# Performance work log

Hardware: AMD Instinct MI355X
Metric: run time of the kernel (lower is better)

The kernel has to match this reference:

```python
import jax, jax.numpy as jnp
import numpy as np

N, E, B = 25600, 307200, 256
H, D, F0, K = 256, 16, 7, 6
GNN_OUT, TDA_IN, TDA_OUT, MEG_IN, MEG_OUT = 192, 32, 128, 16, 64
FUSION = GNN_OUT + TDA_OUT + MEG_OUT  # 384
MID = FUSION // 2  # 192


def _ln(x, g, b, eps=1e-5):
    m = x.mean(-1, keepdims=True)
    v = x.var(-1, keepdims=True)
    return (x - m) * jax.lax.rsqrt(v + eps) * g + b


def _ntn(x, pos, neg):
    return jnp.nan_to_num(x, nan=0.0, posinf=pos, neginf=neg)


def setup_inputs():
    key = jax.random.key(0)
    ks = iter(jax.random.split(key, 80))
    p = lambda *s: 0.05 * jax.random.normal(next(ks), s, jnp.float32)
    inp = {
        "x": jax.random.normal(next(ks), (N, F0), jnp.float32),
        "edge_attr": jax.random.uniform(next(ks), (E, D), dtype=jnp.float32),
        "tda": jax.random.normal(next(ks), (B, TDA_IN), jnp.float32),
        "megnet": jax.random.normal(next(ks), (B, MEG_IN), jnp.float32),
        "edge_index": jax.random.randint(next(ks), (2, E), 0, N),
        "batch": jnp.repeat(jnp.arange(B), N // B),
        # GNN encoder
        "gin_W": p(F0, H), "gin_b": jnp.zeros(H),
        "conv_Wf": p(6, 2 * H + D, H), "conv_bf": jnp.zeros((6, H)),
        "conv_Ws": p(6, 2 * H + D, H), "conv_bs": jnp.zeros((6, H)),
        "gln_g": jnp.ones((6, H)), "gln_b": jnp.zeros((6, H)),
        "gout_W": p(H, GNN_OUT), "gout_b": jnp.zeros(GNN_OUT),
        # TDA projector 32->256->256->128
        "t1_W": p(TDA_IN, 2 * TDA_OUT), "t1_b": jnp.zeros(2 * TDA_OUT),
        "tln1_g": jnp.ones(2 * TDA_OUT), "tln1_b": jnp.zeros(2 * TDA_OUT),
        "t2_W": p(2 * TDA_OUT, 2 * TDA_OUT), "t2_b": jnp.zeros(2 * TDA_OUT),
        "tln2_g": jnp.ones(2 * TDA_OUT), "tln2_b": jnp.zeros(2 * TDA_OUT),
        "t3_W": p(2 * TDA_OUT, TDA_OUT), "t3_b": jnp.zeros(TDA_OUT),
        # MEGNet projector 16->128->128->64
        "m1_W": p(MEG_IN, 2 * MEG_OUT), "m1_b": jnp.zeros(2 * MEG_OUT),
        "mln1_g": jnp.ones(2 * MEG_OUT), "mln1_b": jnp.zeros(2 * MEG_OUT),
        "m2_W": p(2 * MEG_OUT, 2 * MEG_OUT), "m2_b": jnp.zeros(2 * MEG_OUT),
        "mln2_g": jnp.ones(2 * MEG_OUT), "mln2_b": jnp.zeros(2 * MEG_OUT),
        "m3_W": p(2 * MEG_OUT, MEG_OUT), "m3_b": jnp.zeros(MEG_OUT),
        # fusion LN
        "fln_g": jnp.ones(FUSION), "fln_b": jnp.zeros(FUSION),
        # CPPN gate 384->48->24->6
        "g1_W": p(FUSION, K * 8), "g1_b": jnp.zeros(K * 8),
        "hln_g": jnp.ones(K * 8), "hln_b": jnp.zeros(K * 8),
        "g2_W": p(K * 8, K * 4), "g2_b": jnp.zeros(K * 4),
        "g3_W": p(K * 4, K), "g3_b": jnp.zeros(K),
        # CPPN poly branches stacked over K
        "plin_W": p(K, FUSION), "plin_b": jnp.zeros(K),
        "pq1_W": p(K, FUSION, MID), "pq1_b": jnp.zeros((K, MID)),
        "pq2_W": p(K, MID), "pq2_b": jnp.zeros(K),
        "pc1_W": p(K, FUSION, MID // 2), "pc1_b": jnp.zeros((K, MID // 2)),
        "pc2_W": p(K, MID // 2), "pc2_b": jnp.zeros(K),
    }
    return inp


def _forward(x, edge_attr, tda, megnet, edge_index, batch,
             gin_W, gin_b, conv_Wf, conv_bf, conv_Ws, conv_bs, gln_g, gln_b, gout_W, gout_b,
             t1_W, t1_b, tln1_g, tln1_b, t2_W, t2_b, tln2_g, tln2_b, t3_W, t3_b,
             m1_W, m1_b, mln1_g, mln1_b, m2_W, m2_b, mln2_g, mln2_b, m3_W, m3_b,
             fln_g, fln_b,
             g1_W, g1_b, hln_g, hln_b, g2_W, g2_b, g3_W, g3_b,
             plin_W, plin_b, pq1_W, pq1_b, pq2_W, pq2_b, pc1_W, pc1_b, pc2_W, pc2_b):
    silu = jax.nn.silu
    tda = _ntn(tda, 3.0, -3.0)
    megnet = _ntn(megnet, 3.0, -3.0)
    x = _ntn(x, 3.0, -3.0)
    ea = _ntn(edge_attr, 1.0, 0.0)
    src, dst = edge_index[0], edge_index[1]

    h = silu(x @ gin_W + gin_b)  # [N, H]
    for i in range(6):
        # CGConv message: z_ij = [x_i, x_j, e_ij]; sigmoid(z Wf) * softplus(z Ws); sum-agg + root
        z = jnp.concatenate([h[dst], h[src], ea], axis=-1)  # [E, 2H+D]
        msg = jax.nn.sigmoid(z @ conv_Wf[i] + conv_bf[i]) * jax.nn.softplus(z @ conv_Ws[i] + conv_bs[i])
        conv = h + jax.ops.segment_sum(msg, dst, num_segments=N)
        h = _ln(silu(conv) + h, gln_g[i], gln_b[i])
    cnt = jax.ops.segment_sum(jnp.ones((N, 1), h.dtype), batch, num_segments=B)
    pooled = jax.ops.segment_sum(h, batch, num_segments=B) / jnp.maximum(cnt, 1.0)
    z_gnn = jnp.nan_to_num(pooled @ gout_W + gout_b)  # [B, 192]

    # --- projectors ---
    a = _ln(silu(tda @ t1_W + t1_b), tln1_g, tln1_b)
    a = _ln(silu(a @ t2_W + t2_b), tln2_g, tln2_b)
    z_tda = jnp.nan_to_num(a @ t3_W + t3_b)  # [B, 128]
    m = _ln(silu(megnet @ m1_W + m1_b), mln1_g, mln1_b)
    m = _ln(silu(m @ m2_W + m2_b), mln2_g, mln2_b)
    z_meg = jnp.nan_to_num(m @ m3_W + m3_b)  # [B, 64]

    z = _ln(jnp.concatenate([z_gnn, z_tda, z_meg], axis=-1), fln_g, fln_b)  # [B, 384]

    # --- CPPN mixture head ---
    g = _ln(silu(z @ g1_W + g1_b), hln_g, hln_b)
    g = silu(g @ g2_W + g2_b)
    gates = jax.nn.softmax(g @ g3_W + g3_b, axis=-1)  # [B, K]
    lin = jnp.einsum('bd,kd->bk', z, plin_W) + plin_b
    hq = silu(jnp.einsum('bd,kdm->bkm', z, pq1_W) + pq1_b)  # [B, K, 192]
    q = jnp.einsum('bkm,km->bk', hq, pq2_W) + pq2_b
    hc = silu(jnp.einsum('bd,kdm->bkm', z, pc1_W) + pc1_b) ** 2  # [B, K, 96]
    c = jnp.einsum('bkm,km->bk', hc, pc2_W) + pc2_b
    y = (gates * (lin + q + c)).sum(-1)  # [B]
    return y, z


def reference(x, edge_attr, tda, megnet, edge_index, batch,
              gin_W, gin_b, conv_Wf, conv_bf, conv_Ws, conv_bs, gln_g, gln_b, gout_W, gout_b,
              t1_W, t1_b, tln1_g, tln1_b, t2_W, t2_b, tln2_g, tln2_b, t3_W, t3_b,
              m1_W, m1_b, mln1_g, mln1_b, m2_W, m2_b, mln2_g, mln2_b, m3_W, m3_b,
              fln_g, fln_b,
              g1_W, g1_b, hln_g, hln_b, g2_W, g2_b, g3_W, g3_b,
              plin_W, plin_b, pq1_W, pq1_b, pq2_W, pq2_b, pc1_W, pc1_b, pc2_W, pc2_b):
    return _forward(x, edge_attr, tda, megnet, edge_index, batch,
                    gin_W, gin_b, conv_Wf, conv_bf, conv_Ws, conv_bs, gln_g, gln_b, gout_W, gout_b,
                    t1_W, t1_b, tln1_g, tln1_b, t2_W, t2_b, tln2_g, tln2_b, t3_W, t3_b,
                    m1_W, m1_b, mln1_g, mln1_b, m2_W, m2_b, mln2_g, mln2_b, m3_W, m3_b,
                    fln_g, fln_b,
                    g1_W, g1_b, hln_g, hln_b, g2_W, g2_b, g3_W, g3_b,
                    plin_W, plin_b, pq1_W, pq1_b, pq2_W, pq2_b, pc1_W, pc1_b, pc2_W, pc2_b)
```

## Files before the change

### kernel.cpp

```cpp
#include <hip/hip_runtime.h>
#include <hip/hip_bf16.h>
#include <cmath>

#define NN 25600
#define NE 307200
#define NB 256
#define HD 256

typedef __attribute__((ext_vector_type(8))) short short8;
typedef __attribute__((ext_vector_type(4))) float f32x4;
typedef __attribute__((ext_vector_type(2))) float f32x2;

__device__ __forceinline__ float ntn_f(float v, float pos, float neg) {
  if (isnan(v)) return 0.f;
  if (isinf(v)) return v > 0.f ? pos : neg;
  return v;
}
__device__ __forceinline__ float ntn_def(float v) {
  if (isnan(v)) return 0.f;
  if (isinf(v)) return v > 0.f ? 3.4028234663852886e38f : -3.4028234663852886e38f;
  return v;
}
__device__ __forceinline__ float sigmoid_f(float x) { return 1.f / (1.f + __expf(-x)); }
__device__ __forceinline__ float silu_f(float x) { return x * sigmoid_f(x); }
__device__ __forceinline__ float softplus_f(float x) {
  return fmaxf(x, 0.f) + __logf(1.f + __expf(-fabsf(x)));
}
__device__ __forceinline__ unsigned short f2bf(float f) {
  unsigned int u = __float_as_uint(f);
  u += 0x7fffu + ((u >> 16) & 1u);
  return (unsigned short)(u >> 16);
}
__device__ __forceinline__ f32x2 bfpair(unsigned int u) {
  f32x2 r;
  r.x = __uint_as_float(u << 16);
  r.y = __uint_as_float(u & 0xffff0000u);
  return r;
}

template <int NW>
__device__ __forceinline__ float blockSum(float v, float* sred) {
  int lane = threadIdx.x & 63, w = threadIdx.x >> 6;
#pragma unroll
  for (int o = 32; o; o >>= 1) v += __shfl_xor(v, o);
  __syncthreads();
  if (lane == 0) sred[w] = v;
  __syncthreads();
  float r = 0.f;
#pragma unroll
  for (int i = 0; i < NW; ++i) r += sred[i];
  return r;
}

__global__ void k_hist(const int* __restrict__ dst, int* __restrict__ counts, int E) {
  int e = blockIdx.x * 256 + threadIdx.x;
  if (e < E) atomicAdd(&counts[dst[e]], 1);
}

__global__ __launch_bounds__(1024) void k_scan(const int* __restrict__ counts,
                                               int* __restrict__ offs, int n) {
  __shared__ int sd[1024];
  __shared__ int run;
  int tid = threadIdx.x;
  if (tid == 0) run = 0;
  __syncthreads();
  for (int base = 0; base < n; base += 1024) {
    int i = base + tid;
    int v = (i < n) ? counts[i] : 0;
    sd[tid] = v;
    __syncthreads();
    int acc = v;
    for (int off = 1; off < 1024; off <<= 1) {
      int t = (tid >= off) ? sd[tid - off] : 0;
      __syncthreads();
      acc += t;
      sd[tid] = acc;
      __syncthreads();
    }
    int r = run;
    if (i < n) offs[i] = r + acc - v;
    __syncthreads();
    if (tid == 1023) run = r + sd[1023];
    __syncthreads();
  }
  if (threadIdx.x == 0) offs[n] = run;
}

__global__ void k_scatter(const int* __restrict__ dst, const int* __restrict__ offs,
                          int* __restrict__ cursor, int* __restrict__ eidx, int E) {
  int e = blockIdx.x * 256 + threadIdx.x;
  if (e < E) {
    int d = dst[e];
    int p = offs[d] + atomicAdd(&cursor[d], 1);
    eidx[p] = e;
  }
}

__global__ void k_srcperm(const int* __restrict__ eidx, const int* __restrict__ srcArr,
                          int* __restrict__ srcs, int E) {
  int i = blockIdx.x * 256 + threadIdx.x;
  if (i < E) srcs[i] = srcArr[eidx[i]];
}

__global__ void k_eaperm(const int* __restrict__ eidx, const float* __restrict__ ea,
                         float* __restrict__ eacsr, int E) {
  int gid = blockIdx.x * 256 + threadIdx.x;
  if (gid < E * 16) {
    int ii = gid >> 4, k = gid & 15;
    eacsr[gid] = ea[(size_t)eidx[ii] * 16 + k];
  }
}

__global__ void k_pack(const float* __restrict__ conv_Wf, const float* __restrict__ conv_Ws,
                       unsigned short* __restrict__ w4t) {
  int layer = blockIdx.y;
  int gid = blockIdx.x * 256 + threadIdx.x;
  int k = gid & 255;
  int c = gid >> 8;
  int j = c & 255;
  int tbl = c >> 8;
  const float* W = (tbl < 2) ? conv_Wf : conv_Ws;
  int krow = (tbl & 1) ? 256 + k : k;
  float v = W[((size_t)layer * 528 + krow) * 256 + j];
  w4t[((size_t)layer * 1024 + c) * 256 + k] = f2bf(v);
}

__global__ void k_gin(const float* __restrict__ x, const float* __restrict__ W,
                      const float* __restrict__ bias, float* __restrict__ h,
                      unsigned short* __restrict__ hbf) {
  int n = blockIdx.x, j = threadIdx.x;
  float xv[7];
#pragma unroll
  for (int k = 0; k < 7; ++k) xv[k] = ntn_f(x[n * 7 + k], 3.f, -3.f);
  float acc = bias[j];
#pragma unroll
  for (int k = 0; k < 7; ++k) acc += xv[k] * W[k * 256 + j];
  float o = silu_f(acc);
  h[(size_t)n * 256 + j] = o;
  hbf[(size_t)n * 256 + j] = f2bf(o);
}

__global__ __launch_bounds__(256) void k_gemm_bf16(
    const unsigned short* __restrict__ Abf,
    const unsigned short* __restrict__ w4t,
    const float* __restrict__ bf, const float* __restrict__ bs,
    unsigned short* __restrict__ Pout) {
  __shared__ unsigned short As[128 * 56];
  __shared__ unsigned short Bs[128 * 56];
  int tid = threadIdx.x;
  int lane = tid & 63, w = tid >> 6;
  int wr = w >> 1, wc = w & 1;
  int m0 = blockIdx.x * 128, n0 = blockIdx.y * 128;
  int l15 = lane & 15, l4 = lane >> 4;
  f32x4 acc[4][4];
#pragma unroll
  for (int i = 0; i < 4; ++i)
#pragma unroll
    for (int j = 0; j < 4; ++j) acc[i][j] = (f32x4)0.f;
  for (int kt = 0; kt < 8; ++kt) {
    int k0 = kt * 32;
    if (kt) __syncthreads();
#pragma unroll
    for (int c = 0; c < 2; ++c) {
      int chunk = tid + c * 256;
      int row = chunk >> 2, q = chunk & 3;
      *(uint4*)&As[row * 56 + q * 8] =
          *(const uint4*)&Abf[(size_t)(m0 + row) * 256 + k0 + q * 8];
      *(uint4*)&Bs[row * 56 + q * 8] =
          *(const uint4*)&w4t[(size_t)(n0 + row) * 256 + k0 + q * 8];
    }
    __syncthreads();
    short8 a[4], b[4];
#pragma unroll
    for (int f = 0; f < 4; ++f) {
      a[f] = *(const short8*)&As[(wr * 64 + f * 16 + l15) * 56 + l4 * 8];
      b[f] = *(const short8*)&Bs[(wc * 64 + f * 16 + l15) * 56 + l4 * 8];
    }
#pragma unroll
    for (int i = 0; i < 4; ++i)
#pragma unroll
      for (int j = 0; j < 4; ++j)
        acc[i][j] = __builtin_amdgcn_mfma_f32_16x16x32_bf16(a[i], b[j], acc[i][j], 0, 0, 0);
  }
#pragma unroll
  for (int j = 0; j < 4; ++j) {
    int gcol = n0 + wc * 64 + j * 16 + l15;
    float bias = (gcol < 256) ? bf[gcol] : (gcol >= 512 && gcol < 768) ? bs[gcol - 512] : 0.f;
#pragma unroll
    for (int i = 0; i < 4; ++i) {
#pragma unroll
      for (int r = 0; r < 4; ++r) {
        int grow = m0 + wr * 64 + i * 16 + l4 * 4 + r;
        Pout[(size_t)grow * 1024 + gcol] = f2bf(acc[i][j][r] + bias);
      }
    }
  }
}

__global__ __launch_bounds__(256, 2) void k_edge(
    const float* __restrict__ h, const unsigned short* __restrict__ P,
    const float* __restrict__ eacsr,
    const int* __restrict__ srcs, const int* __restrict__ offs,
    const float* __restrict__ WfE, const float* __restrict__ WsE,
    const float* __restrict__ lng, const float* __restrict__ lnb,
    float* __restrict__ hout, unsigned short* __restrict__ hbfout) {
  __shared__ float sr1[4], sr2[4];
  int tid = threadIdx.x;
  int lane = tid & 63;
  int w = tid >> 6;
  int n = blockIdx.x * 2 + (w >> 1);
  int half = w & 1;
  int idx = half * 128 + lane * 2;
  f32x2 wf2[16], ws2[16];
#pragma unroll
  for (int k = 0; k < 16; ++k) {
    wf2[k] = *(const f32x2*)(WfE + k * 256 + idx);
    ws2[k] = *(const f32x2*)(WsE + k * 256 + idx);
  }
  f32x2 lg = *(const f32x2*)(lng + idx);
  f32x2 lb = *(const f32x2*)(lnb + idx);

  const unsigned short* Pn = P + (size_t)n * 1024;
  f32x2 pfd = bfpair(*(const unsigned int*)(Pn + idx));
  f32x2 psd = bfpair(*(const unsigned int*)(Pn + 512 + idx));
  f32x2 hn = *(const f32x2*)(h + (size_t)n * 256 + idx);
  f32x2 acc = (f32x2)0.f;
  int e0 = __builtin_amdgcn_readfirstlane(offs[n]);
  int e1 = __builtin_amdgcn_readfirstlane(offs[n + 1]);

  for (int ii = e0; ii < e1; ++ii) {
    int s = srcs[ii];
    const unsigned short* Ps = P + (size_t)s * 1024;
    unsigned int uf = *(const unsigned int*)(Ps + 256 + idx);
    unsigned int us = *(const unsigned int*)(Ps + 768 + idx);
    float carr[16];
    const float4* ea4 = (const float4*)(eacsr + ((size_t)ii << 4));
    *(float4*)&carr[0] = ea4[0];
    *(float4*)&carr[4] = ea4[1];
    *(float4*)&carr[8] = ea4[2];
    *(float4*)&carr[12] = ea4[3];
    f32x2 af = pfd, as_ = psd;
#pragma unroll
    for (int k = 0; k < 16; ++k) {
      float c = carr[k];
      af += c * wf2[k];
      as_ += c * ws2[k];
    }
    af += bfpair(uf);
    as_ += bfpair(us);
    acc.x += sigmoid_f(af.x) * softplus_f(as_.x);
    acc.y += sigmoid_f(af.y) * softplus_f(as_.y);
  }
  float cv0 = hn.x + acc.x;
  float cv1 = hn.y + acc.y;
  float t0 = silu_f(cv0) + hn.x;
  float t1 = silu_f(cv1) + hn.y;
  float s1 = t0 + t1, s2 = t0 * t0 + t1 * t1;
#pragma unroll
  for (int o = 32; o; o >>= 1) {
    s1 += __shfl_xor(s1, o);
    s2 += __shfl_xor(s2, o);
  }
  if (lane == 0) { sr1[w] = s1; sr2[w] = s2; }
  __syncthreads();
  int pw = w ^ 1;
  float S1 = sr1[w] + sr1[pw];
  float S2 = sr2[w] + sr2[pw];
  float mean = S1 * (1.f / 256.f);
  float var = S2 * (1.f / 256.f) - mean * mean;
  float inv = rsqrtf(var + 1e-5f);
  float o0 = (t0 - mean) * inv * lg.x + lb.x;
  float o1 = (t1 - mean) * inv * lg.y + lb.y;
  f32x2 ov; ov.x = o0; ov.y = o1;
  *(f32x2*)(hout + (size_t)n * 256 + idx) = ov;
  unsigned int pk = (unsigned int)f2bf(o0) | ((unsigned int)f2bf(o1) << 16);
  *(unsigned int*)(hbfout + (size_t)n * 256 + idx) = pk;
}

__global__ __launch_bounds__(256) void k_pool2(const float* __restrict__ h,
                                               float* __restrict__ pooled) {
  int b = blockIdx.x, j = threadIdx.x;
  const float* hp = h + (size_t)b * 100 * 256 + j;
  float s = 0.f;
  for (int i = 0; i < 100; ++i) s += hp[(size_t)i * 256];
  pooled[b * 256 + j] = s * 0.01f;
}

__global__ void k_zgnn(const float* __restrict__ pooled,
                       const float* __restrict__ W, const float* __restrict__ bias,
                       float* __restrict__ zf) {
  int b = blockIdx.x, j = threadIdx.x;
  float acc = bias[j];
  for (int k = 0; k < 256; ++k) acc += pooled[b * 256 + k] * W[k * 192 + j];
  zf[b * 384 + j] = ntn_def(acc);
}

__global__ __launch_bounds__(256) void k_tda(const float* __restrict__ tda,
    const float* __restrict__ W1, const float* __restrict__ b1,
    const float* __restrict__ g1, const float* __restrict__ bb1,
    const float* __restrict__ W2, const float* __restrict__ b2,
    const float* __restrict__ g2, const float* __restrict__ bb2,
    const float* __restrict__ W3, const float* __restrict__ b3, float* __restrict__ zf) {
  __shared__ float sin_[32];
  __shared__ float sa[256];
  __shared__ float sred[4];
  int b = blockIdx.x, tid = threadIdx.x;
  if (tid < 32) sin_[tid] = ntn_f(tda[b * 32 + tid], 3.f, -3.f);
  __syncthreads();
  float v = b1[tid];
#pragma unroll
  for (int k = 0; k < 32; ++k) v += sin_[k] * W1[k * 256 + tid];
  v = silu_f(v);
  float s1 = blockSum<4>(v, sred);
  float s2 = blockSum<4>(v * v, sred);
  float mean = s1 * (1.f / 256.f), var = s2 * (1.f / 256.f) - mean * mean;
  float inv = rsqrtf(var + 1e-5f);
  v = (v - mean) * inv * g1[tid] + bb1[tid];
  sa[tid] = v;
  __syncthreads();
  float v2 = b2[tid];
  for (int k = 0; k < 256; ++k) v2 += sa[k] * W2[k * 256 + tid];
  v2 = silu_f(v2);
  s1 = blockSum<4>(v2, sred);
  s2 = blockSum<4>(v2 * v2, sred);
  mean = s1 * (1.f / 256.f); var = s2 * (1.f / 256.f) - mean * mean;
  inv = rsqrtf(var + 1e-5f);
  v2 = (v2 - mean) * inv * g2[tid] + bb2[tid];
  __syncthreads();
  sa[tid] = v2;
  __syncthreads();
  if (tid < 128) {
    float o = b3[tid];
    for (int k = 0; k < 256; ++k) o += sa[k] * W3[k * 128 + tid];
    zf[b * 384 + 192 + tid] = ntn_def(o);
  }
}

__global__ __launch_bounds__(128) void k_meg(const float* __restrict__ mg,
    const float* __restrict__ W1, const float* __restrict__ b1,
    const float* __restrict__ g1, const float* __restrict__ bb1,
    const float* __restrict__ W2, const float* __restrict__ b2,
    const float* __restrict__ g2, const float* __restrict__ bb2,
    const float* __restrict__ W3, const float* __restrict__ b3, float* __restrict__ zf) {
  __shared__ float sin_[16];
  __shared__ float sa[128];
  __shared__ float sred[2];
  int b = blockIdx.x, tid = threadIdx.x;
  if (tid < 16) sin_[tid] = ntn_f(mg[b * 16 + tid], 3.f, -3.f);
  __syncthreads();
  float v = b1[tid];
#pragma unroll
  for (int k = 0; k < 16; ++k) v += sin_[k] * W1[k * 128 + tid];
  v = silu_f(v);
  float s1 = blockSum<2>(v, sred);
  float s2 = blockSum<2>(v * v, sred);
  float mean = s1 * (1.f / 128.f), var = s2 * (1.f / 128.f) - mean * mean;
  float inv = rsqrtf(var + 1e-5f);
  v = (v - mean) * inv * g1[tid] + bb1[tid];
  sa[tid] = v;
  __syncthreads();
  float v2 = b2[tid];
  for (int k = 0; k < 128; ++k) v2 += sa[k] * W2[k * 128 + tid];
  v2 = silu_f(v2);
  s1 = blockSum<2>(v2, sred);
  s2 = blockSum<2>(v2 * v2, sred);
  mean = s1 * (1.f / 128.f); var = s2 * (1.f / 128.f) - mean * mean;
  inv = rsqrtf(var + 1e-5f);
  v2 = (v2 - mean) * inv * g2[tid] + bb2[tid];
  __syncthreads();
  sa[tid] = v2;
  __syncthreads();
  if (tid < 64) {
    float o = b3[tid];
    for (int k = 0; k < 128; ++k) o += sa[k] * W3[k * 64 + tid];
    zf[b * 384 + 320 + tid] = ntn_def(o);
  }
}

__global__ __launch_bounds__(384) void k_cppn(const float* __restrict__ zf,
    const float* __restrict__ flng, const float* __restrict__ flnb,
    const float* __restrict__ g1W, const float* __restrict__ g1b,
    const float* __restrict__ hg, const float* __restrict__ hb,
    const float* __restrict__ g2W, const float* __restrict__ g2b,
    const float* __restrict__ g3W, const float* __restrict__ g3b,
    const float* __restrict__ plW, const float* __restrict__ plb,
    const float* __restrict__ pq1W, const float* __restrict__ pq1b,
    const float* __restrict__ pq2W, const float* __restrict__ pq2b,
    const float* __restrict__ pc1W, const float* __restrict__ pc1b,
    const float* __restrict__ pc2W, const float* __restrict__ pc2b,
    float* __restrict__ zout, float* __restrict__ y) {
  __shared__ float sz[384];
  __shared__ float sred[6];
  __shared__ float sg[48];
  __shared__ float s24[24];
  __shared__ float gates[6];
  __shared__ float lin[6];
  __shared__ float qv[6], cvv[6];
  __shared__ float mn48, iv48;
  __shared__ float prodq[1152];
  __shared__ float prodc[576];
  int b = blockIdx.x, tid = threadIdx.x;
  int lane = tid & 63, wv = tid >> 6;

  float v = zf[(size_t)b * 384 + tid];
  float s1 = blockSum<6>(v, sred);
  float s2 = blockSum<6>(v * v, sred);
  float mean = s1 * (1.f / 384.f), var = s2 * (1.f / 384.f) - mean * mean;
  float inv = rsqrtf(var + 1e-5f);
  float zv = (v - mean) * inv * flng[tid] + flnb[tid];
  sz[tid] = zv;
  zout[(size_t)b * 384 + tid] = zv;
  __syncthreads();

  {
    int j = tid >> 3, p = tid & 7;
    float a = 0.f;
    for (int d = p; d < 384; d += 8) a += sz[d] * g1W[d * 48 + j];
    a += __shfl_xor(a, 1);
    a += __shfl_xor(a, 2);
    a += __shfl_xor(a, 4);
    if (p == 0) sg[j] = silu_f(a + g1b[j]);
  }
  __syncthreads();
  if (tid < 64) {
    float x = (tid < 48) ? sg[tid] : 0.f;
    float t1 = x, t2 = x * x;
#pragma unroll
    for (int o = 32; o; o >>= 1) {
      t1 += __shfl_xor(t1, o);
      t2 += __shfl_xor(t2, o);
    }
    if (tid == 0) {
      mn48 = t1 * (1.f / 48.f);
      float vr = t2 * (1.f / 48.f) - mn48 * mn48;
      iv48 = rsqrtf(vr + 1e-5f);
    }
  }
  __syncthreads();
  if (tid < 48) sg[tid] = (sg[tid] - mn48) * iv48 * hg[tid] + hb[tid];
  __syncthreads();
  {
    int j = tid >> 4, p = tid & 15;
    int d0 = p * 3;
    float a = sg[d0] * g2W[d0 * 24 + j] + sg[d0 + 1] * g2W[(d0 + 1) * 24 + j] +
              sg[d0 + 2] * g2W[(d0 + 2) * 24 + j];
    a += __shfl_xor(a, 1);
    a += __shfl_xor(a, 2);
    a += __shfl_xor(a, 4);
    a += __shfl_xor(a, 8);
    if (p == 0) s24[j] = silu_f(a + g2b[j]);
  }
  __syncthreads();
  if (tid < 6) {
    float a = g3b[tid];
    for (int k = 0; k < 24; ++k) a += s24[k] * g3W[k * 6 + tid];
    gates[tid] = a;
  }
  __syncthreads();
  if (tid == 0) {
    float mx = gates[0];
    for (int i = 1; i < 6; ++i) mx = fmaxf(mx, gates[i]);
    float s = 0.f;
    for (int i = 0; i < 6; ++i) { gates[i] = __expf(gates[i] - mx); s += gates[i]; }
    float rs = 1.f / s;
    for (int i = 0; i < 6; ++i) gates[i] *= rs;
  }
  {
    float p = 0.f;
    for (int d = lane; d < 384; d += 64) p += sz[d] * plW[wv * 384 + d];
#pragma unroll
    for (int o = 32; o; o >>= 1) p += __shfl_xor(p, o);
    if (lane == 0) lin[wv] = p + plb[wv];
  }
  if (tid < 288) {
    int k = tid / 48, m4 = (tid % 48) * 4;
    f32x4 a = (f32x4)0.f;
    const float* Wp = pq1W + (size_t)k * 384 * 192 + m4;
    for (int d = 0; d < 384; ++d) {
      float4 w4 = *(const float4*)(Wp + (size_t)d * 192);
      float zd = sz[d];
      a.x += zd * w4.x; a.y += zd * w4.y; a.z += zd * w4.z; a.w += zd * w4.w;
    }
#pragma unroll
    for (int r = 0; r < 4; ++r) {
      int m = m4 + r;
      prodq[k * 192 + m] = silu_f(a[r] + pq1b[k * 192 + m]) * pq2W[k * 192 + m];
    }
  }
  if (tid < 144) {
    int k = tid / 24, m4 = (tid % 24) * 4;
    f32x4 a = (f32x4)0.f;
    const float* Wp = pc1W + (size_t)k * 384 * 96 + m4;
    for (int d = 0; d < 384; ++d) {
      float4 w4 = *(const float4*)(Wp + (size_t)d * 96);
      float zd = sz[d];
      a.x += zd * w4.x; a.y += zd * w4.y; a.z += zd * w4.z; a.w += zd * w4.w;
    }
#pragma unroll
    for (int r = 0; r < 4; ++r) {
      int m = m4 + r;
      float sl = silu_f(a[r] + pc1b[k * 96 + m]);
      prodc[k * 96 + m] = sl * sl * pc2W[k * 96 + m];
    }
  }
  __syncthreads();
  {
    float s = prodq[wv * 192 + lane] + prodq[wv * 192 + 64 + lane] +
              prodq[wv * 192 + 128 + lane];
#pragma unroll
    for (int o = 32; o; o >>= 1) s += __shfl_xor(s, o);
    if (lane == 0) qv[wv] = s + pq2b[wv];
    float c = prodc[wv * 96 + lane];
    float c2 = (lane < 32) ? prodc[wv * 96 + 64 + lane] : 0.f;
    float sc = c + c2;
#pragma unroll
    for (int o = 32; o; o >>= 1) sc += __shfl_xor(sc, o);
    if (lane == 0) cvv[wv] = sc + pc2b[wv];
  }
  __syncthreads();
  if (tid == 0) {
    float yy = 0.f;
    for (int k = 0; k < 6; ++k) yy += gates[k] * (lin[k] + qv[k] + cvv[k]);
    y[b] = yy;
  }
}

extern "C" void kernel_launch(void* const* d_in, const int* in_sizes, int n_in,
                              void* d_out, int out_size, void* d_ws, size_t ws_size,
                              hipStream_t stream) {
  const float* x         = (const float*)d_in[0];
  const float* edge_attr = (const float*)d_in[1];
  const float* tda       = (const float*)d_in[2];
  const float* megnet    = (const float*)d_in[3];
  const int*   edge_index= (const int*)d_in[4];
  const float* gin_W = (const float*)d_in[6];
  const float* gin_b = (const float*)d_in[7];
  const float* conv_Wf = (const float*)d_in[8];
  const float* conv_bf = (const float*)d_in[9];
  const float* conv_Ws = (const float*)d_in[10];
  const float* conv_bs = (const float*)d_in[11];
  const float* gln_g = (const float*)d_in[12];
  const float* gln_b = (const float*)d_in[13];
  const float* gout_W = (const float*)d_in[14];
  const float* gout_b = (const float*)d_in[15];
  const float* t1_W = (const float*)d_in[16];
  const float* t1_b = (const float*)d_in[17];
  const float* tln1_g = (const float*)d_in[18];
  const float* tln1_b = (const float*)d_in[19];
  const float* t2_W = (const float*)d_in[20];
  const float* t2_b = (const float*)d_in[21];
  const float* tln2_g = (const float*)d_in[22];
  const float* tln2_b = (const float*)d_in[23];
  const float* t3_W = (const float*)d_in[24];
  const float* t3_b = (const float*)d_in[25];
  const float* m1_W = (const float*)d_in[26];
  const float* m1_b = (const float*)d_in[27];
  const float* mln1_g = (const float*)d_in[28];
  const float* mln1_b = (const float*)d_in[29];
  const float* m2_W = (const float*)d_in[30];
  const float* m2_b = (const float*)d_in[31];
  const float* mln2_g = (const float*)d_in[32];
  const float* mln2_b = (const float*)d_in[33];
  const float* m3_W = (const float*)d_in[34];
  const float* m3_b = (const float*)d_in[35];
  const float* fln_g = (const float*)d_in[36];
  const float* fln_b = (const float*)d_in[37];
  const float* g1_W = (const float*)d_in[38];
  const float* g1_b = (const float*)d_in[39];
  const float* hln_g = (const float*)d_in[40];
  const float* hln_b = (const float*)d_in[41];
  const float* g2_W = (const float*)d_in[42];
  const float* g2_b = (const float*)d_in[43];
  const float* g3_W = (const float*)d_in[44];
  const float* g3_b = (const float*)d_in[45];
  const float* plin_W = (const float*)d_in[46];
  const float* plin_b = (const float*)d_in[47];
  const float* pq1_W = (const float*)d_in[48];
  const float* pq1_b = (const float*)d_in[49];
  const float* pq2_W = (const float*)d_in[50];
  const float* pq2_b = (const float*)d_in[51];
  const float* pc1_W = (const float*)d_in[52];
  const float* pc1_b = (const float*)d_in[53];
  const float* pc2_W = (const float*)d_in[54];
  const float* pc2_b = (const float*)d_in[55];

  float* ws = (float*)d_ws;
  float* hA = ws;
  float* hB = hA + (size_t)NN * 256;
  float* pooled = hB + (size_t)NN * 256;
  float* zf = pooled + (size_t)NB * 256;
  float* eacsr = zf + (size_t)NB * 384;
  unsigned short* hbfA = (unsigned short*)(eacsr + (size_t)NE * 16);
  unsigned short* hbfB = hbfA + (size_t)NN * 256;
  unsigned short* Pbf = hbfB + (size_t)NN * 256;
  unsigned short* w4t = Pbf + (size_t)NN * 1024;
  int* counts = (int*)(w4t + (size_t)6 * 1024 * 256);
  int* cursor = counts + NN;
  int* offs = cursor + NN;
  int* eidx = offs + NN + 1;
  int* srcs = eidx + NE;

  const int* srcArr = edge_index;
  const int* dstArr = edge_index + NE;

  hipMemsetAsync(counts, 0, (size_t)2 * NN * sizeof(int), stream);

  k_hist<<<(NE + 255) / 256, 256, 0, stream>>>(dstArr, counts, NE);
  k_scan<<<1, 1024, 0, stream>>>(counts, offs, NN);
  k_scatter<<<(NE + 255) / 256, 256, 0, stream>>>(dstArr, offs, cursor, eidx, NE);
  k_srcperm<<<(NE + 255) / 256, 256, 0, stream>>>(eidx, srcArr, srcs, NE);
  k_eaperm<<<(NE * 16 + 255) / 256, 256, 0, stream>>>(eidx, edge_attr, eacsr, NE);
  k_pack<<<dim3(1024, 6), 256, 0, stream>>>(conv_Wf, conv_Ws, w4t);

  k_gin<<<NN, 256, 0, stream>>>(x, gin_W, gin_b, hA, hbfA);

  float* hcur = hA;          float* hnext = hB;
  unsigned short* bcur = hbfA; unsigned short* bnext = hbfB;
  for (int i = 0; i < 6; ++i) {
    const float* Wf = conv_Wf + (size_t)i * 528 * 256;
    const float* Ws = conv_Ws + (size_t)i * 528 * 256;
    k_gemm_bf16<<<dim3(NN / 128, 8), 256, 0, stream>>>(
        bcur, w4t + (size_t)i * 1024 * 256, conv_bf + i * 256, conv_bs + i * 256, Pbf);
    k_edge<<<NN / 2, 256, 0, stream>>>(hcur, Pbf, eacsr, srcs, offs,
                                       Wf + 512 * 256, Ws + 512 * 256,
                                       gln_g + i * 256, gln_b + i * 256, hnext, bnext);
    float* tf = hcur; hcur = hnext; hnext = tf;
    unsigned short* tb = bcur; bcur = bnext; bnext = tb;
  }

  k_pool2<<<NB, 256, 0, stream>>>(hcur, pooled);
  k_zgnn<<<NB, 192, 0, stream>>>(pooled, gout_W, gout_b, zf);
  k_tda<<<NB, 256, 0, stream>>>(tda, t1_W, t1_b, tln1_g, tln1_b, t2_W, t2_b, tln2_g, tln2_b,
                                t3_W, t3_b, zf);
  k_meg<<<NB, 128, 0, stream>>>(megnet, m1_W, m1_b, mln1_g, mln1_b, m2_W, m2_b, mln2_g, mln2_b,
                                m3_W, m3_b, zf);

  float* yout = (float*)d_out;
  float* zout = yout + NB;
  k_cppn<<<NB, 384, 0, stream>>>(zf, fln_g, fln_b,
                                 g1_W, g1_b, hln_g, hln_b, g2_W, g2_b, g3_W, g3_b,
                                 plin_W, plin_b, pq1_W, pq1_b, pq2_W, pq2_b,
                                 pc1_W, pc1_b, pc2_W, pc2_b, zout, yout);
}
```

Measured before the change: 1.361 ms.

## Precompute edge-attribute projections via MFMA GEMM and simplify edge kernel

Adds a per-layer bf16 MFMA GEMM that projects padded edge attributes through the edge-feature slices of the gate and message weights into a large per-edge buffer. A new edge kernel then just gathers and adds these precomputed terms, four nodes per block, instead of doing 16 FMAs per edge per channel. This removes edge-loop arithmetic and register pressure but adds a large per-layer materialised tensor with heavy memory traffic and bf16 rounding of the edge term. The path is gated on workspace size, with fallback to the old kernel.

```diff
diff --git a/kernel.cpp b/kernel.cpp
--- a/kernel.cpp
+++ b/kernel.cpp
@@ -111,6 +111,16 @@
   }
 }
 
+__global__ void k_eapermb(const int* __restrict__ eidx, const float* __restrict__ ea,
+                          unsigned short* __restrict__ eab, int E) {
+  int gid = blockIdx.x * 256 + threadIdx.x;
+  if (gid < E * 32) {
+    int ii = gid >> 5, k = gid & 31;
+    float v = (k < 16) ? ea[(size_t)eidx[ii] * 16 + k] : 0.f;
+    eab[gid] = f2bf(v);
+  }
+}
+
 __global__ void k_pack(const float* __restrict__ conv_Wf, const float* __restrict__ conv_Ws,
                        unsigned short* __restrict__ w4t) {
   int layer = blockIdx.y;
@@ -123,6 +133,17 @@
   int krow = (tbl & 1) ? 256 + k : k;
   float v = W[((size_t)layer * 528 + krow) * 256 + j];
   w4t[((size_t)layer * 1024 + c) * 256 + k] = f2bf(v);
+}
+
+__global__ void k_packE(const float* __restrict__ conv_Wf, const float* __restrict__ conv_Ws,
+                        unsigned short* __restrict__ wet) {
+  int layer = blockIdx.y;
+  int gid = blockIdx.x * 256 + threadIdx.x;
+  int k = gid & 31, c = gid >> 5;
+  const float* W = (c < 256) ? conv_Wf : conv_Ws;
+  int j = c & 255;
+  float v = (k < 16) ? W[((size_t)layer * 528 + 512 + k) * 256 + j] : 0.f;
+  wet[((size_t)layer * 512 + c) * 32 + k] = f2bf(v);
 }
 
 __global__ void k_gin(const float* __restrict__ x, const float* __restrict__ W,
@@ -195,6 +216,120 @@
       }
     }
   }
+}
+
+__global__ __launch_bounds__(256) void k_gemm_eaf(
+    const unsigned short* __restrict__ Ab,
+    const unsigned short* __restrict__ Bt,
+    unsigned short* __restrict__ C) {
+  __shared__ unsigned short As[128 * 40];
+  __shared__ unsigned short Bs[128 * 40];
+  int tid = threadIdx.x;
+  int lane = tid & 63, w = tid >> 6;
+  int wr = w >> 1, wc = w & 1;
+  int m0 = blockIdx.x * 128, n0 = blockIdx.y * 128;
+  int l15 = lane & 15, l4 = lane >> 4;
+#pragma unroll
+  for (int c = 0; c < 2; ++c) {
+    int chunk = tid + c * 256;
+    int row = chunk >> 2, q = chunk & 3;
+    *(uint4*)&As[row * 40 + q * 8] = *(const uint4*)&Ab[(size_t)(m0 + row) * 32 + q * 8];
+    *(uint4*)&Bs[row * 40 + q * 8] = *(const uint4*)&Bt[(size_t)(n0 + row) * 32 + q * 8];
+  }
+  __syncthreads();
+  short8 a[4], b[4];
+#pragma unroll
+  for (int f = 0; f < 4; ++f) {
+    a[f] = *(const short8*)&As[(wr * 64 + f * 16 + l15) * 40 + l4 * 8];
+    b[f] = *(const short8*)&Bs[(wc * 64 + f * 16 + l15) * 40 + l4 * 8];
+  }
+  f32x4 acc[4][4];
+#pragma unroll
+  for (int i = 0; i < 4; ++i)
+#pragma unroll
+    for (int j = 0; j < 4; ++j)
+      acc[i][j] = __builtin_amdgcn_mfma_f32_16x16x32_bf16(a[i], b[j], (f32x4)0.f, 0, 0, 0);
+#pragma unroll
+  for (int j = 0; j < 4; ++j) {
+    int gcol = n0 + wc * 64 + j * 16 + l15;
+#pragma unroll
+    for (int i = 0; i < 4; ++i) {
+#pragma unroll
+      for (int r = 0; r < 4; ++r) {
+        int grow = m0 + wr * 64 + i * 16 + l4 * 4 + r;
+        C[(size_t)grow * 512 + gcol] = f2bf(acc[i][j][r]);
+      }
+    }
+  }
+}
+
+__global__ __launch_bounds__(256) void k_edge2(
+    const float* __restrict__ h, const unsigned short* __restrict__ P,
+    const unsigned short* __restrict__ EAF,
+    const int* __restrict__ srcs, const int* __restrict__ offs,
+    const float* __restrict__ lng, const float* __restrict__ lnb,
+    float* __restrict__ hout, unsigned short* __restrict__ hbfout) {
+  int lane = threadIdx.x & 63;
+  int n = blockIdx.x * 4 + (threadIdx.x >> 6);
+  int idx = lane * 4;
+  float4 g4 = *(const float4*)(lng + idx);
+  float4 b4 = *(const float4*)(lnb + idx);
+  const unsigned short* Pn = P + (size_t)n * 1024;
+  uint2 ud0 = *(const uint2*)(Pn + idx);
+  uint2 ud1 = *(const uint2*)(Pn + 512 + idx);
+  f32x2 pfd0 = bfpair(ud0.x), pfd1 = bfpair(ud0.y);
+  f32x2 psd0 = bfpair(ud1.x), psd1 = bfpair(ud1.y);
+  float4 hn4 = *(const float4*)(h + (size_t)n * 256 + idx);
+  float acc[4] = {0.f, 0.f, 0.f, 0.f};
+  int e0 = __builtin_amdgcn_readfirstlane(offs[n]);
+  int e1 = __builtin_amdgcn_readfirstlane(offs[n + 1]);
+
+  for (int ii = e0; ii < e1; ++ii) {
+    int s = srcs[ii];
+    const unsigned short* Ps = P + (size_t)s * 1024;
+    uint2 uf = *(const uint2*)(Ps + 256 + idx);
+    uint2 us = *(const uint2*)(Ps + 768 + idx);
+    const unsigned short* Ee = EAF + (size_t)ii * 512;
+    uint2 ef = *(const uint2*)(Ee + idx);
+    uint2 es = *(const uint2*)(Ee + 256 + idx);
+    f32x2 af0 = pfd0 + bfpair(uf.x) + bfpair(ef.x);
+    f32x2 af1 = pfd1 + bfpair(uf.y) + bfpair(ef.y);
+    f32x2 as0 = psd0 + bfpair(us.x) + bfpair(es.x);
+    f32x2 as1 = psd1 + bfpair(us.y) + bfpair(es.y);
+    acc[0] += sigmoid_f(af0.x) * softplus_f(as0.x);
+    acc[1] += sigmoid_f(af0.y) * softplus_f(as0.y);
+    acc[2] += sigmoid_f(af1.x) * softplus_f(as1.x);
+    acc[3] += sigmoid_f(af1.y) * softplus_f(as1.y);
+  }
+  float hv[4] = {hn4.x, hn4.y, hn4.z, hn4.w};
+  float t[4], s1 = 0.f, s2 = 0.f;
+#pragma unroll
+  for (int q = 0; q < 4; ++q) {
+    float cv = hv[q] + acc[q];
+    t[q] = silu_f(cv) + hv[q];
+    s1 += t[q];
+    s2 += t[q] * t[q];
+  }
+#pragma unroll
+  for (int o = 32; o; o >>= 1) {
+    s1 += __shfl_xor(s1, o);
+    s2 += __shfl_xor(s2, o);
+  }
+  float mean = s1 * (1.f / 256.f);
+  float var = s2 * (1.f / 256.f) - mean * mean;
+  float inv = rsqrtf(var + 1e-5f);
+  float gg[4] = {g4.x, g4.y, g4.z, g4.w};
+  float bb[4] = {b4.x, b4.y, b4.z, b4.w};
+  float o0 = (t[0] - mean) * inv * gg[0] + bb[0];
+  float o1 = (t[1] - mean) * inv * gg[1] + bb[1];
+  float o2 = (t[2] - mean) * inv * gg[2] + bb[2];
+  float o3 = (t[3] - mean) * inv * gg[3] + bb[3];
+  float4 o4v; o4v.x = o0; o4v.y = o1; o4v.z = o2; o4v.w = o3;
+  *(float4*)(hout + (size_t)n * 256 + idx) = o4v;
+  uint2 pk;
+  pk.x = (unsigned int)f2bf(o0) | ((unsigned int)f2bf(o1) << 16);
+  pk.y = (unsigned int)f2bf(o2) | ((unsigned int)f2bf(o3) << 16);
+  *(uint2*)(hbfout + (size_t)n * 256 + idx) = pk;
 }
 
 __global__ __launch_bounds__(256, 2) void k_edge(
@@ -219,7 +354,6 @@
   }
   f32x2 lg = *(const f32x2*)(lng + idx);
   f32x2 lb = *(const f32x2*)(lnb + idx);
-
   const unsigned short* Pn = P + (size_t)n * 1024;
   f32x2 pfd = bfpair(*(const unsigned int*)(Pn + idx));
   f32x2 psd = bfpair(*(const unsigned int*)(Pn + 512 + idx));
@@ -227,7 +361,6 @@
   f32x2 acc = (f32x2)0.f;
   int e0 = __builtin_amdgcn_readfirstlane(offs[n]);
   int e1 = __builtin_amdgcn_readfirstlane(offs[n + 1]);
-
   for (int ii = e0; ii < e1; ++ii) {
     int s = srcs[ii];
     const unsigned short* Ps = P + (size_t)s * 1024;
@@ -594,11 +727,18 @@
   unsigned short* hbfB = hbfA + (size_t)NN * 256;
   unsigned short* Pbf = hbfB + (size_t)NN * 256;
   unsigned short* w4t = Pbf + (size_t)NN * 1024;
-  int* counts = (int*)(w4t + (size_t)6 * 1024 * 256);
+  unsigned short* wet = w4t + (size_t)6 * 1024 * 256;
+  unsigned short* eab = wet + (size_t)6 * 512 * 32;
+  int* counts = (int*)(eab + (size_t)NE * 32);
   int* cursor = counts + NN;
   int* offs = cursor + NN;
   int* eidx = offs + NN + 1;
   int* srcs = eidx + NE;
+  size_t off_bytes = (size_t)((char*)(srcs + NE) - (char*)d_ws);
+  off_bytes = (off_bytes + 255) & ~(size_t)255;
+  unsigned short* EAF = (unsigned short*)((char*)d_ws + off_bytes);
+  size_t need = off_bytes + (size_t)NE * 512 * 2;
+  bool useEAF = (ws_size >= need);
 
   const int* srcArr = edge_index;
   const int* dstArr = edge_index + NE;
@@ -609,8 +749,13 @@
   k_scan<<<1, 1024, 0, stream>>>(counts, offs, NN);
   k_scatter<<<(NE + 255) / 256, 256, 0, stream>>>(dstArr, offs, cursor, eidx, NE);
   k_srcperm<<<(NE + 255) / 256, 256, 0, stream>>>(eidx, srcArr, srcs, NE);
-  k_eaperm<<<(NE * 16 + 255) / 256, 256, 0, stream>>>(eidx, edge_attr, eacsr, NE);
   k_pack<<<dim3(1024, 6), 256, 0, stream>>>(conv_Wf, conv_Ws, w4t);
+  if (useEAF) {
+    k_eapermb<<<(NE * 32 + 255) / 256, 256, 0, stream>>>(eidx, edge_attr, eab, NE);
+    k_packE<<<dim3(64, 6), 256, 0, stream>>>(conv_Wf, conv_Ws, wet);
+  } else {
+    k_eaperm<<<(NE * 16 + 255) / 256, 256, 0, stream>>>(eidx, edge_attr, eacsr, NE);
+  }
 
   k_gin<<<NN, 256, 0, stream>>>(x, gin_W, gin_b, hA, hbfA);
 
@@ -621,9 +766,15 @@
     const float* Ws = conv_Ws + (size_t)i * 528 * 256;
     k_gemm_bf16<<<dim3(NN / 128, 8), 256, 0, stream>>>(
         bcur, w4t + (size_t)i * 1024 * 256, conv_bf + i * 256, conv_bs + i * 256, Pbf);
-    k_edge<<<NN / 2, 256, 0, stream>>>(hcur, Pbf, eacsr, srcs, offs,
-                                       Wf + 512 * 256, Ws + 512 * 256,
-                                       gln_g + i * 256, gln_b + i * 256, hnext, bnext);
+    if (useEAF) {
+      k_gemm_eaf<<<dim3(NE / 128, 4), 256, 0, stream>>>(eab, wet + (size_t)i * 512 * 32, EAF);
+      k_edge2<<<NN / 4, 256, 0, stream>>>(hcur, Pbf, EAF, srcs, offs,
+                                          gln_g + i * 256, gln_b + i * 256, hnext, bnext);
+    } else {
+      k_edge<<<NN / 2, 256, 0, stream>>>(hcur, Pbf, eacsr, srcs, offs,
+                                         Wf + 512 * 256, Ws + 512 * 256,
+                                         gln_g + i * 256, gln_b + i * 256, hnext, bnext);
+    }
     float* tf = hcur; hcur = hnext; hnext = tf;
     unsigned short* tb = bcur; bcur = bnext; bnext = tb;
   }
```

Result: no change. 1.363 ms (+0.1%).

## Use packed fp16 dot products for edge-attribute projection in edge kernel

Applied to the files above, without the earlier changes.

Edge attributes and the 16-row edge weight slices are pre-packed into fp16 pairs, and the per-edge projection uses v_dot2 fp16 instructions instead of 32 scalar FMAs per output pair. This halves edge-attribute bandwidth per edge (32 bytes instead of 64) and cuts ALU work and weight registers in the hot gather loop. The occupancy hint of 2 blocks per SM is dropped. It adds an fp16 rounding error on the edge features and weights.

```diff
diff --git a/kernel.cpp b/kernel.cpp
--- a/kernel.cpp
+++ b/kernel.cpp
@@ -10,6 +10,8 @@
 typedef __attribute__((ext_vector_type(8))) short short8;
 typedef __attribute__((ext_vector_type(4))) float f32x4;
 typedef __attribute__((ext_vector_type(2))) float f32x2;
+typedef __attribute__((ext_vector_type(2))) _Float16 h16x2;
+typedef __attribute__((ext_vector_type(2))) __fp16 fp16x2;
 
 __device__ __forceinline__ float ntn_f(float v, float pos, float neg) {
   if (isnan(v)) return 0.f;
@@ -31,12 +33,24 @@
   u += 0x7fffu + ((u >> 16) & 1u);
   return (unsigned short)(u >> 16);
 }
-__device__ __forceinline__ f32x2 bfpair(unsigned int u) {
-  f32x2 r;
-  r.x = __uint_as_float(u << 16);
-  r.y = __uint_as_float(u & 0xffff0000u);
-  return r;
-}
+__device__ __forceinline__ float bflo(unsigned int u) { return __uint_as_float(u << 16); }
+__device__ __forceinline__ float bfhi(unsigned int u) { return __uint_as_float(u & 0xffff0000u); }
+__device__ __forceinline__ h16x2 u2h(unsigned int u) {
+  union { unsigned int u; h16x2 h; } x; x.u = u; return x.h;
+}
+__device__ __forceinline__ unsigned int pk2u(float a, float b) {
+  union { fp16x2 p; unsigned int u; } x;
+  x.p = __builtin_amdgcn_cvt_pkrtz(a, b);
+  return x.u;
+}
+#if __has_builtin(__builtin_amdgcn_fdot2)
+#define FDOT2(a, b, c) __builtin_amdgcn_fdot2((a), (b), (c), false)
+#else
+__device__ __forceinline__ float fdot2_sw(h16x2 a, h16x2 b, float c) {
+  return (float)a.x * (float)b.x + (float)a.y * (float)b.y + c;
+}
+#define FDOT2(a, b, c) fdot2_sw((a), (b), (c))
+#endif
 
 template <int NW>
 __device__ __forceinline__ float blockSum(float v, float* sred) {
@@ -102,12 +116,15 @@
   if (i < E) srcs[i] = srcArr[eidx[i]];
 }
 
-__global__ void k_eaperm(const int* __restrict__ eidx, const float* __restrict__ ea,
-                         float* __restrict__ eacsr, int E) {
+__global__ void k_eapermh(const int* __restrict__ eidx, const float* __restrict__ ea,
+                          unsigned int* __restrict__ eah, int E) {
   int gid = blockIdx.x * 256 + threadIdx.x;
-  if (gid < E * 16) {
-    int ii = gid >> 4, k = gid & 15;
-    eacsr[gid] = ea[(size_t)eidx[ii] * 16 + k];
+  if (gid < E * 8) {
+    int ii = gid >> 3, kp = gid & 7;
+    int e = eidx[ii];
+    float v0 = ea[(size_t)e * 16 + 2 * kp];
+    float v1 = ea[(size_t)e * 16 + 2 * kp + 1];
+    eah[gid] = pk2u(v0, v1);
   }
 }
 
@@ -123,6 +140,19 @@
   int krow = (tbl & 1) ? 256 + k : k;
   float v = W[((size_t)layer * 528 + krow) * 256 + j];
   w4t[((size_t)layer * 1024 + c) * 256 + k] = f2bf(v);
+}
+
+__global__ void k_packEh(const float* __restrict__ conv_Wf, const float* __restrict__ conv_Ws,
+                         unsigned int* __restrict__ wh) {
+  int layer = blockIdx.y;
+  int gid = blockIdx.x * 256 + threadIdx.x;
+  int dp = gid >> 5, dw = gid & 31;
+  int g = dw >> 4, dloc = (dw >> 3) & 1, kp = dw & 7;
+  int d = dp * 2 + dloc;
+  const float* W = g ? conv_Ws : conv_Wf;
+  float v0 = W[((size_t)layer * 528 + 512 + 2 * kp) * 256 + d];
+  float v1 = W[((size_t)layer * 528 + 512 + 2 * kp + 1) * 256 + d];
+  wh[((size_t)layer * 128 + dp) * 32 + dw] = pk2u(v0, v1);
 }
 
 __global__ void k_gin(const float* __restrict__ x, const float* __restrict__ W,
@@ -197,34 +227,42 @@
   }
 }
 
-__global__ __launch_bounds__(256, 2) void k_edge(
+__global__ __launch_bounds__(256) void k_edge3(
     const float* __restrict__ h, const unsigned short* __restrict__ P,
-    const float* __restrict__ eacsr,
+    const unsigned int* __restrict__ eah,
     const int* __restrict__ srcs, const int* __restrict__ offs,
-    const float* __restrict__ WfE, const float* __restrict__ WsE,
+    const unsigned int* __restrict__ wh,
     const float* __restrict__ lng, const float* __restrict__ lnb,
     float* __restrict__ hout, unsigned short* __restrict__ hbfout) {
   __shared__ float sr1[4], sr2[4];
-  int tid = threadIdx.x;
-  int lane = tid & 63;
-  int w = tid >> 6;
+  int tid = threadIdx.x, lane = tid & 63, w = tid >> 6;
   int n = blockIdx.x * 2 + (w >> 1);
   int half = w & 1;
   int idx = half * 128 + lane * 2;
-  f32x2 wf2[16], ws2[16];
-#pragma unroll
-  for (int k = 0; k < 16; ++k) {
-    wf2[k] = *(const f32x2*)(WfE + k * 256 + idx);
-    ws2[k] = *(const f32x2*)(WsE + k * 256 + idx);
-  }
+  int dp = half * 64 + lane;
+
+  unsigned int wk[32];
+  {
+    const uint4* wb = (const uint4*)(wh + (size_t)dp * 32);
+#pragma unroll
+    for (int q = 0; q < 8; ++q) {
+      uint4 t = wb[q];
+      wk[q * 4 + 0] = t.x; wk[q * 4 + 1] = t.y;
+      wk[q * 4 + 2] = t.z; wk[q * 4 + 3] = t.w;
+    }
+  }
+#pragma unroll
+  for (int q = 0; q < 32; ++q) asm volatile("" : "+v"(wk[q]));
+
   f32x2 lg = *(const f32x2*)(lng + idx);
   f32x2 lb = *(const f32x2*)(lnb + idx);
-
   const unsigned short* Pn = P + (size_t)n * 1024;
-  f32x2 pfd = bfpair(*(const unsigned int*)(Pn + idx));
-  f32x2 psd = bfpair(*(const unsigned int*)(Pn + 512 + idx));
+  unsigned int ud0 = *(const unsigned int*)(Pn + idx);
+  unsigned int ud1 = *(const unsigned int*)(Pn + 512 + idx);
+  float pf0 = bflo(ud0), pf1 = bfhi(ud0);
+  float ps0 = bflo(ud1), ps1 = bfhi(ud1);
   f32x2 hn = *(const f32x2*)(h + (size_t)n * 256 + idx);
-  f32x2 acc = (f32x2)0.f;
+  float acc0 = 0.f, acc1 = 0.f;
   int e0 = __builtin_amdgcn_readfirstlane(offs[n]);
   int e1 = __builtin_amdgcn_readfirstlane(offs[n + 1]);
 
@@ -233,26 +271,25 @@
     const unsigned short* Ps = P + (size_t)s * 1024;
     unsigned int uf = *(const unsigned int*)(Ps + 256 + idx);
     unsigned int us = *(const unsigned int*)(Ps + 768 + idx);
-    float carr[16];
-    const float4* ea4 = (const float4*)(eacsr + ((size_t)ii << 4));
-    *(float4*)&carr[0] = ea4[0];
-    *(float4*)&carr[4] = ea4[1];
-    *(float4*)&carr[8] = ea4[2];
-    *(float4*)&carr[12] = ea4[3];
-    f32x2 af = pfd, as_ = psd;
-#pragma unroll
-    for (int k = 0; k < 16; ++k) {
-      float c = carr[k];
-      af += c * wf2[k];
-      as_ += c * ws2[k];
-    }
-    af += bfpair(uf);
-    as_ += bfpair(us);
-    acc.x += sigmoid_f(af.x) * softplus_f(as_.x);
-    acc.y += sigmoid_f(af.y) * softplus_f(as_.y);
-  }
-  float cv0 = hn.x + acc.x;
-  float cv1 = hn.y + acc.y;
+    const uint4* e4 = (const uint4*)(eah + (size_t)ii * 8);
+    uint4 ea0 = e4[0], ea1 = e4[1];
+    unsigned int ec[8] = {ea0.x, ea0.y, ea0.z, ea0.w, ea1.x, ea1.y, ea1.z, ea1.w};
+    float af0 = pf0, af1 = pf1, as0 = ps0, as1 = ps1;
+#pragma unroll
+    for (int kp = 0; kp < 8; ++kp) {
+      h16x2 c = u2h(ec[kp]);
+      af0 = FDOT2(u2h(wk[kp]), c, af0);
+      af1 = FDOT2(u2h(wk[8 + kp]), c, af1);
+      as0 = FDOT2(u2h(wk[16 + kp]), c, as0);
+      as1 = FDOT2(u2h(wk[24 + kp]), c, as1);
+    }
+    af0 += bflo(uf); af1 += bfhi(uf);
+    as0 += bflo(us); as1 += bfhi(us);
+    acc0 += sigmoid_f(af0) * softplus_f(as0);
+    acc1 += sigmoid_f(af1) * softplus_f(as1);
+  }
+  float cv0 = hn.x + acc0;
+  float cv1 = hn.y + acc1;
   float t0 = silu_f(cv0) + hn.x;
   float t1 = silu_f(cv1) + hn.y;
   float s1 = t0 + t1, s2 = t0 * t0 + t1 * t1;
@@ -589,12 +626,13 @@
   float* hB = hA + (size_t)NN * 256;
   float* pooled = hB + (size_t)NN * 256;
   float* zf = pooled + (size_t)NB * 256;
-  float* eacsr = zf + (size_t)NB * 384;
-  unsigned short* hbfA = (unsigned short*)(eacsr + (size_t)NE * 16);
+  unsigned short* hbfA = (unsigned short*)(zf + (size_t)NB * 384);
   unsigned short* hbfB = hbfA + (size_t)NN * 256;
   unsigned short* Pbf = hbfB + (size_t)NN * 256;
   unsigned short* w4t = Pbf + (size_t)NN * 1024;
-  int* counts = (int*)(w4t + (size_t)6 * 1024 * 256);
+  unsigned int* wh6 = (unsigned int*)(w4t + (size_t)6 * 1024 * 256);
+  unsigned int* eah = wh6 + (size_t)6 * 128 * 32;
+  int* counts = (int*)(eah + (size_t)NE * 8);
   int* cursor = counts + NN;
   int* offs = cursor + NN;
   int* eidx = offs + NN + 1;
@@ -609,21 +647,20 @@
   k_scan<<<1, 1024, 0, stream>>>(counts, offs, NN);
   k_scatter<<<(NE + 255) / 256, 256, 0, stream>>>(dstArr, offs, cursor, eidx, NE);
   k_srcperm<<<(NE + 255) / 256, 256, 0, stream>>>(eidx, srcArr, srcs, NE);
-  k_eaperm<<<(NE * 16 + 255) / 256, 256, 0, stream>>>(eidx, edge_attr, eacsr, NE);
+  k_eapermh<<<(NE * 8 + 255) / 256, 256, 0, stream>>>(eidx, edge_attr, eah, NE);
   k_pack<<<dim3(1024, 6), 256, 0, stream>>>(conv_Wf, conv_Ws, w4t);
+  k_packEh<<<dim3(16, 6), 256, 0, stream>>>(conv_Wf, conv_Ws, wh6);
 
   k_gin<<<NN, 256, 0, stream>>>(x, gin_W, gin_b, hA, hbfA);
 
   float* hcur = hA;          float* hnext = hB;
   unsigned short* bcur = hbfA; unsigned short* bnext = hbfB;
   for (int i = 0; i < 6; ++i) {
-    const float* Wf = conv_Wf + (size_t)i * 528 * 256;
-    const float* Ws = conv_Ws + (size_t)i * 528 * 256;
     k_gemm_bf16<<<dim3(NN / 128, 8), 256, 0, stream>>>(
         bcur, w4t + (size_t)i * 1024 * 256, conv_bf + i * 256, conv_bs + i * 256, Pbf);
-    k_edge<<<NN / 2, 256, 0, stream>>>(hcur, Pbf, eacsr, srcs, offs,
-                                       Wf + 512 * 256, Ws + 512 * 256,
-                                       gln_g + i * 256, gln_b + i * 256, hnext, bnext);
+    k_edge3<<<NN / 2, 256, 0, stream>>>(hcur, Pbf, eah, srcs, offs,
+                                        wh6 + (size_t)i * 128 * 32,
+                                        gln_g + i * 256, gln_b + i * 256, hnext, bnext);
     float* tf = hcur; hcur = hnext; hnext = tf;
     unsigned short* tb = bcur; bcur = bnext; bnext = tb;
   }
```

Result: faster. 1.323 ms (-2.8%).
